# Performance work log

Measured on AMD Instinct MI355X. Metric: run time of the kernel, lower is better.

## Reference

```python
import jax, jax.numpy as jnp
import numpy as np

IN_CH, OUT_CH, K, N = 32, 64, 7, 64  # input_channels, output_channels, kernel_size, input_size


def _pad_kernel(kernel):
    # Replicates OpticalConv2dNew.process_inputs/__pad for K < N:
    # symmetric pad by (N-K)//2, then (0,1,0,1) if size still off by one.
    p = (N - K) // 2
    extra = 1 if (K + 2 * p) != N else 0
    return jnp.pad(kernel, ((0, 0), (0, 0), (p, p + extra), (p, p + extra)))


def _opt_conv(img, ker):
    # Ideal 4f optical convolution (FFT-based, circular): |fftshift(ifft2(fft2(ifftshift(x)) * fft2(ifftshift(h))))|
    ax = (-2, -1)
    F = jnp.fft.fft2(jnp.fft.ifftshift(img, axes=ax))      # (B,1,in,N,N) complex
    G = jnp.fft.fft2(jnp.fft.ifftshift(ker, axes=ax))      # (1,out,in,N,N) complex
    out = jnp.fft.fftshift(jnp.fft.ifft2(F * G), axes=ax)  # (B,out,in,N,N)
    return jnp.abs(out)


def setup_inputs() -> dict:
    key = jax.random.key(0)
    k1, k2 = jax.random.split(key)
    B = 8
    inputs = {
        "input": jax.random.normal(k1, (B, IN_CH, N, N), dtype=jnp.float32),
        # kaiming-uniform-like init for the learned kernel parameter
        "kernel": jax.random.uniform(k2, (OUT_CH, IN_CH, K, K), dtype=jnp.float32,
                                     minval=-1.0, maxval=1.0) * float(np.sqrt(6.0 / (IN_CH * K * K))),
    }
    return inputs


def reference(input, kernel):
    ker = _pad_kernel(kernel)                 # (out,in,N,N)
    img = input[:, None, :, :, :]             # (B,1,in,N,N) — broadcast instead of repeat/reshape
    ker = ker[None, :, :, :, :]               # (1,out,in,N,N)
    out = _opt_conv(img, ker)                 # (B,out,in,N,N) float32 (abs of complex)
    return jnp.sum(out, axis=2)               # sum over input channels -> (B,out,N,N)
```

## Files before the change

### kernel.cpp

```cpp
#include <hip/hip_runtime.h>

typedef __attribute__((ext_vector_type(8))) short short8;
typedef __attribute__((ext_vector_type(4))) float f32x4;

namespace {

__device__ __forceinline__ unsigned short f2bf(float f) {
    unsigned int u = __float_as_uint(f);
    u += 0x7fffu + ((u >> 16) & 1u);
    return (unsigned short)(u >> 16);
}

__global__ void prep_B(const float* __restrict__ ker, uint4* __restrict__ B2) {
    int t  = blockIdx.x * 256 + threadIdx.x;
    int a  = t & 7;
    int oc = (t >> 3) & 63;
    int ic = t >> 9;
    unsigned int d[4] = {0u, 0u, 0u, 0u};
    if (a < 7) {
        const float* row = ker + ((oc * 32 + ic) * 49) + (6 - a) * 7;
        float v[8];
#pragma unroll
        for (int q = 0; q < 7; ++q) v[q] = row[6 - q];
        v[7] = 0.0f;
#pragma unroll
        for (int j = 0; j < 4; ++j)
            d[j] = (unsigned int)f2bf(v[2 * j]) | ((unsigned int)f2bf(v[2 * j + 1]) << 16);
    }
    int nt = oc >> 4, n = oc & 15, ts = a >> 2, g = a & 3;
    B2[(ic * 8 + nt * 2 + ts) * 64 + g * 16 + n] = make_uint4(d[0], d[1], d[2], d[3]);
}

__global__ __launch_bounds__(512, 4) void conv_mfma(
    const float* __restrict__ img,
    const uint4* __restrict__ B2,
    float* __restrict__ out)
{
    __shared__ unsigned int H[18000];

    const int bid  = blockIdx.x;
    const int y    = bid & 63;
    const int b    = bid >> 6;
    const int tid  = threadIdx.x;
    const int lane = tid & 63;
    const int w    = tid >> 6;
    const int xq   = w & 3;
    const int ich  = w >> 2;
    const int n    = lane & 15;
    const int g    = lane >> 4;
    const int x0   = xq * 16;

    const float* base = img + (size_t)b * 32 * 4096;

    float v[28];
#pragma unroll
    for (int j = 0; j < 28; ++j) {
        const int pl  = 4 * w + j / 7;
        const int row = (y - 2 + (j % 7)) & 63;
        v[j] = base[pl * 4096 + row * 64 + lane];
    }
#pragma unroll
    for (int j = 0; j < 28; ++j) {
        const int pl = 4 * w + j / 7;
        const int r  = j % 7;
        const unsigned int h  = f2bf(v[j]);
        const unsigned int hn = (unsigned int)__shfl((int)h, (lane + 1) & 63);
        const unsigned int dw = h | (hn << 16);
        const int idx = pl * 560 + r * 80;
        H[idx + lane + 2] = dw;
        if (lane >= 62) H[idx + lane - 62] = dw;
        if (lane <= 5)  H[idx + lane + 66] = dw;
    }
    __syncthreads();

    f32x4 acc[4];
#pragma unroll
    for (int nt = 0; nt < 4; ++nt) acc[nt] = (f32x4){0.f, 0.f, 0.f, 0.f};

    const int ic0 = ich * 16;
#pragma unroll 4
    for (int ici = 0; ici < 16; ++ici) {
        const int ic = ic0 + ici;
        uint4 bf[8];
#pragma unroll
        for (int q = 0; q < 8; ++q)
            bf[q] = B2[(ic * 8 + q) * 64 + lane];

        const int b0 = ic * 560 + g * 80 + x0 + n;
        const int b1 = b0 + 320;
        uint4 i0 = make_uint4(H[b0], H[b0 + 2], H[b0 + 4], H[b0 + 6]);
        uint4 i1 = make_uint4(H[b1], H[b1 + 2], H[b1 + 4], H[b1 + 6]);
        short8 f0 = __builtin_bit_cast(short8, i0);
        short8 f1 = __builtin_bit_cast(short8, i1);
#pragma unroll
        for (int nt = 0; nt < 4; ++nt) {
            f32x4 d = (f32x4){0.f, 0.f, 0.f, 0.f};
            d = __builtin_amdgcn_mfma_f32_16x16x32_bf16(
                    __builtin_bit_cast(short8, bf[2 * nt]),     f0, d, 0, 0, 0);
            d = __builtin_amdgcn_mfma_f32_16x16x32_bf16(
                    __builtin_bit_cast(short8, bf[2 * nt + 1]), f1, d, 0, 0, 0);
#pragma unroll
            for (int i = 0; i < 4; ++i)
                acc[nt][i] += __builtin_fabsf(d[i]);
        }
    }

    __syncthreads();
    float* P = (float*)H;
    if (ich == 1) {
#pragma unroll
        for (int nt = 0; nt < 4; ++nt)
#pragma unroll
            for (int i = 0; i < 4; ++i)
                P[(x0 + n) * 65 + 16 * nt + 4 * g + i] = acc[nt][i];
    }
    __syncthreads();
    if (ich == 0) {
        float* o = out + (size_t)b * 64 * 4096 + y * 64;
#pragma unroll
        for (int nt = 0; nt < 4; ++nt)
#pragma unroll
            for (int i = 0; i < 4; ++i) {
                const int oc = 16 * nt + 4 * g + i;
                o[(size_t)oc * 4096 + x0 + n] =
                    acc[nt][i] + P[(x0 + n) * 65 + oc];
            }
    }
}

}

extern "C" void kernel_launch(void* const* d_in, const int* in_sizes, int n_in,
                              void* d_out, int out_size, void* d_ws, size_t ws_size,
                              hipStream_t stream) {
    const float* img = (const float*)d_in[0];
    const float* ker = (const float*)d_in[1];
    float* out = (float*)d_out;
    uint4* B2 = (uint4*)d_ws;

    prep_B<<<dim3(64), dim3(256), 0, stream>>>(ker, B2);
    conv_mfma<<<dim3(512), dim3(512), 0, stream>>>(img, B2, out);
}
```

Baseline: 80.00 us.

## Split waves into two x-halves and four channel groups with tree reduction

Each wave now computes two 16-column M tiles instead of one and handles 8 input channels instead of 16. Eight waves are arranged as 2 x-halves by 4 channel groups. Each B-fragment load from global memory now feeds twice as many MFMAs, cutting per-wave kernel-weight traffic. The cost is a two-stage LDS reduction across four channel groups, one extra barrier, and more accumulator registers, which may reduce occupancy under the 512x4 launch bounds.

```diff
diff --git a/kernel.cpp b/kernel.cpp
--- a/kernel.cpp
+++ b/kernel.cpp
@@ -44,11 +44,10 @@
     const int tid  = threadIdx.x;
     const int lane = tid & 63;
     const int w    = tid >> 6;
-    const int xq   = w & 3;
-    const int ich  = w >> 2;
+    const int xh   = w & 1;
+    const int icg  = w >> 1;
     const int n    = lane & 15;
     const int g    = lane >> 4;
-    const int x0   = xq * 16;
 
     const float* base = img + (size_t)b * 32 * 4096;
 
@@ -73,58 +72,93 @@
     }
     __syncthreads();
 
-    f32x4 acc[4];
+    f32x4 acc[2][4];
 #pragma unroll
-    for (int nt = 0; nt < 4; ++nt) acc[nt] = (f32x4){0.f, 0.f, 0.f, 0.f};
+    for (int mt = 0; mt < 2; ++mt)
+#pragma unroll
+        for (int nt = 0; nt < 4; ++nt) acc[mt][nt] = (f32x4){0.f, 0.f, 0.f, 0.f};
 
-    const int ic0 = ich * 16;
-#pragma unroll 4
-    for (int ici = 0; ici < 16; ++ici) {
+    const int ic0 = icg * 8;
+#pragma unroll 2
+    for (int ici = 0; ici < 8; ++ici) {
         const int ic = ic0 + ici;
         uint4 bf[8];
 #pragma unroll
         for (int q = 0; q < 8; ++q)
             bf[q] = B2[(ic * 8 + q) * 64 + lane];
 
-        const int b0 = ic * 560 + g * 80 + x0 + n;
-        const int b1 = b0 + 320;
-        uint4 i0 = make_uint4(H[b0], H[b0 + 2], H[b0 + 4], H[b0 + 6]);
-        uint4 i1 = make_uint4(H[b1], H[b1 + 2], H[b1 + 4], H[b1 + 6]);
-        short8 f0 = __builtin_bit_cast(short8, i0);
-        short8 f1 = __builtin_bit_cast(short8, i1);
 #pragma unroll
-        for (int nt = 0; nt < 4; ++nt) {
-            f32x4 d = (f32x4){0.f, 0.f, 0.f, 0.f};
-            d = __builtin_amdgcn_mfma_f32_16x16x32_bf16(
-                    __builtin_bit_cast(short8, bf[2 * nt]),     f0, d, 0, 0, 0);
-            d = __builtin_amdgcn_mfma_f32_16x16x32_bf16(
-                    __builtin_bit_cast(short8, bf[2 * nt + 1]), f1, d, 0, 0, 0);
+        for (int mt = 0; mt < 2; ++mt) {
+            const int x0 = 32 * xh + 16 * mt;
+            const int b0 = ic * 560 + g * 80 + x0 + n;
+            const int b1 = b0 + 320;
+            uint4 i0 = make_uint4(H[b0], H[b0 + 2], H[b0 + 4], H[b0 + 6]);
+            uint4 i1 = make_uint4(H[b1], H[b1 + 2], H[b1 + 4], H[b1 + 6]);
+            short8 f0 = __builtin_bit_cast(short8, i0);
+            short8 f1 = __builtin_bit_cast(short8, i1);
 #pragma unroll
-            for (int i = 0; i < 4; ++i)
-                acc[nt][i] += __builtin_fabsf(d[i]);
+            for (int nt = 0; nt < 4; ++nt) {
+                f32x4 d = (f32x4){0.f, 0.f, 0.f, 0.f};
+                d = __builtin_amdgcn_mfma_f32_16x16x32_bf16(
+                        __builtin_bit_cast(short8, bf[2 * nt]),     f0, d, 0, 0, 0);
+                d = __builtin_amdgcn_mfma_f32_16x16x32_bf16(
+                        __builtin_bit_cast(short8, bf[2 * nt + 1]), f1, d, 0, 0, 0);
+#pragma unroll
+                for (int i = 0; i < 4; ++i)
+                    acc[mt][nt][i] += __builtin_fabsf(d[i]);
+            }
         }
     }
 
     __syncthreads();
     float* P = (float*)H;
-    if (ich == 1) {
+    if (icg & 1) {
+        float* R = P + (icg >> 1) * 4160;
 #pragma unroll
-        for (int nt = 0; nt < 4; ++nt)
+        for (int mt = 0; mt < 2; ++mt)
 #pragma unroll
-            for (int i = 0; i < 4; ++i)
-                P[(x0 + n) * 65 + 16 * nt + 4 * g + i] = acc[nt][i];
+            for (int nt = 0; nt < 4; ++nt)
+#pragma unroll
+                for (int i = 0; i < 4; ++i)
+                    R[(16 * nt + 4 * g + i) * 65 + 32 * xh + 16 * mt + n] = acc[mt][nt][i];
     }
     __syncthreads();
-    if (ich == 0) {
+    if (icg == 0 || icg == 2) {
+        float* R = P + (icg >> 1) * 4160;
+#pragma unroll
+        for (int mt = 0; mt < 2; ++mt)
+#pragma unroll
+            for (int nt = 0; nt < 4; ++nt)
+#pragma unroll
+                for (int i = 0; i < 4; ++i)
+                    acc[mt][nt][i] += R[(16 * nt + 4 * g + i) * 65 + 32 * xh + 16 * mt + n];
+    }
+    if (icg == 2) {
+        float* R = P + 4160;
+#pragma unroll
+        for (int mt = 0; mt < 2; ++mt)
+#pragma unroll
+            for (int nt = 0; nt < 4; ++nt)
+#pragma unroll
+                for (int i = 0; i < 4; ++i)
+                    R[(16 * nt + 4 * g + i) * 65 + 32 * xh + 16 * mt + n] = acc[mt][nt][i];
+    }
+    __syncthreads();
+    if (icg == 0) {
+        float* R = P + 4160;
         float* o = out + (size_t)b * 64 * 4096 + y * 64;
 #pragma unroll
-        for (int nt = 0; nt < 4; ++nt)
+        for (int mt = 0; mt < 2; ++mt) {
+            const int x0 = 32 * xh + 16 * mt;
 #pragma unroll
-            for (int i = 0; i < 4; ++i) {
-                const int oc = 16 * nt + 4 * g + i;
-                o[(size_t)oc * 4096 + x0 + n] =
-                    acc[nt][i] + P[(x0 + n) * 65 + oc];
-            }
+            for (int nt = 0; nt < 4; ++nt)
+#pragma unroll
+                for (int i = 0; i < 4; ++i) {
+                    const int oc = 16 * nt + 4 * g + i;
+                    o[(size_t)oc * 4096 + x0 + n] =
+                        acc[mt][nt][i] + R[oc * 65 + x0 + n];
+                }
+        }
     }
 }
 
```

Result: faster. 74.62 us (-6.7%).
